# Kernel optimization log

Hardware: AMD Instinct MI355X
Metric: run time of the kernel (lower is better)

Reference implementation:

```python
import jax, jax.numpy as jnp
import numpy as np

N_HEAD = 16


def setup_inputs() -> dict:
    key = jax.random.key(0)
    ks = jax.random.split(key, 5)
    B, S, D = 4, 2048, 1024
    scale = 1.0 / np.sqrt(D)
    return {
        "x": jax.random.normal(ks[0], (B, S, D), dtype=jnp.float32),
        "Wq": jax.random.normal(ks[1], (D, D), dtype=jnp.float32) * scale,
        "bq": jnp.zeros((D,), dtype=jnp.float32),
        "Wk": jax.random.normal(ks[2], (D, D), dtype=jnp.float32) * scale,
        "bk": jnp.zeros((D,), dtype=jnp.float32),
        "Wv": jax.random.normal(ks[3], (D, D), dtype=jnp.float32) * scale,
        "bv": jnp.zeros((D,), dtype=jnp.float32),
        "Wo": jax.random.normal(ks[4], (D, D), dtype=jnp.float32) * scale,
        "bo": jnp.zeros((D,), dtype=jnp.float32),
    }


def reference(x, Wq, bq, Wk, bk, Wv, bv, Wo, bo):
    B, S, D = x.shape
    H = N_HEAD
    Dh = D // H
    # projections (torch Linear == x @ W^T + b; here W stored as (in, out))
    q = (x @ Wq + bq).reshape(B, S, H, Dh).transpose(0, 2, 1, 3)  # (B,H,S,Dh)
    k = (x @ Wk + bk).reshape(B, S, H, Dh).transpose(0, 2, 1, 3)
    v = (x @ Wv + bv).reshape(B, S, H, Dh).transpose(0, 2, 1, 3)
    scores = jnp.einsum("bhsd,bhtd->bhst", q, k) / jnp.sqrt(jnp.float32(Dh))
    causal = jnp.tril(jnp.ones((S, S), dtype=bool))  # (S,S)
    scores = jnp.where(causal[None, None], scores, -jnp.inf)
    weights = jax.nn.softmax(scores, axis=-1)  # (B,H,S,S)
    attn = jnp.einsum("bhst,bhtd->bhsd", weights, v)
    attn = attn.transpose(0, 2, 1, 3).reshape(B, S, D)
    out = attn @ Wo + bo
    return out
```

## Files before the change

### kernel.cpp

```cpp
#include <hip/hip_runtime.h>
#include <hip/hip_bf16.h>


typedef __bf16 bf16x8 __attribute__((ext_vector_type(8)));
typedef float f32x4 __attribute__((ext_vector_type(4)));
typedef unsigned short u16;

__device__ __forceinline__ u16 f2b(float f) {
    __hip_bfloat16 h = __float2bfloat16(f);
    return __builtin_bit_cast(unsigned short, h);
}

__device__ __forceinline__ f32x4 mfma16(bf16x8 a, bf16x8 b, f32x4 c) {
    return __builtin_amdgcn_mfma_f32_16x16x32_bf16(a, b, c, 0, 0, 0);
}

typedef const __attribute__((address_space(1))) unsigned int* gas1_t;
typedef __attribute__((address_space(3))) unsigned int* las3_t;
__device__ __forceinline__ void gld16(const void* g, void* l) {
    __builtin_amdgcn_global_load_lds((gas1_t)g, (las3_t)l, 16, 0, 0);
}

__global__ __launch_bounds__(256) void convert_x(const float* __restrict__ x,
                                                 u16* __restrict__ xb, int n4) {
    int i = blockIdx.x * 256 + threadIdx.x;
    if (i < n4) {
        float4 v = ((const float4*)x)[i];
        ushort4 u;
        u.x = f2b(v.x); u.y = f2b(v.y); u.z = f2b(v.z); u.w = f2b(v.w);
        ((ushort4*)xb)[i] = u;
    }
}

__global__ __launch_bounds__(256) void transpose_w(const float* __restrict__ Wq,
                                                   const float* __restrict__ Wk,
                                                   const float* __restrict__ Wv,
                                                   const float* __restrict__ Wo,
                                                   u16* __restrict__ wqkvt,
                                                   u16* __restrict__ wot) {
    const int z = blockIdx.z;
    const float* src = (z == 0) ? Wq : (z == 1) ? Wk : (z == 2) ? Wv : Wo;
    u16* dst = (z == 3) ? wot : (wqkvt + (size_t)z * 1024 * 1024);
    __shared__ float tile[32][33];
    const int tx = threadIdx.x, ty = threadIdx.y;
    const int nbase = blockIdx.x * 32, kbase = blockIdx.y * 32;
    for (int j = 0; j < 4; ++j)
        tile[ty + j * 8][tx] = src[(size_t)(kbase + ty + j * 8) * 1024 + nbase + tx];
    __syncthreads();
    for (int j = 0; j < 4; ++j)
        dst[(size_t)(nbase + ty + j * 8) * 1024 + kbase + tx] = f2b(tile[tx][ty + j * 8]);
}

__global__ __launch_bounds__(256) void pack_bqkv(const float* __restrict__ bq,
                                                 const float* __restrict__ bk,
                                                 const float* __restrict__ bv,
                                                 float* __restrict__ bqkv) {
    int i = blockIdx.x * 256 + threadIdx.x;
    bqkv[i] = (i < 1024) ? bq[i] : (i < 2048) ? bk[i - 1024] : bv[i - 2048];
}

__global__ __launch_bounds__(512, 2) void gemm256(const u16* __restrict__ A,
                                                  const u16* __restrict__ Bt,
                                                  const float* __restrict__ bias,
                                                  u16* __restrict__ qkout,
                                                  u16* __restrict__ vtout,
                                                  int K) {
    const int tid = threadIdx.x;
    const int l = tid & 63;
    const int w = tid >> 6;
    const int mw = w >> 1;
    const int nw = w & 1;
    const int mrow = l & 15;
    const int tileM = blockIdx.x * 256;
    const int tileN = blockIdx.y * 256;

    __shared__ u16 As[2][2][256 * 32];
    __shared__ u16 Bs[2][2][256 * 32];

    const int rco = ((l >> 4) ^ ((l >> 1) & 3)) * 8;

    const int srow = l >> 2;
    const int scg = (l & 3) ^ ((l >> 3) & 3);
    const u16* aSt = A + (size_t)(tileM + w * 16 + srow) * K + scg * 8;
    const u16* bSt = Bt + (size_t)(tileN + w * 16 + srow) * K + scg * 8;

    f32x4 acc[4][8] = {};

    auto stageAB = [&](int ks, int tt, int nb) {
        const size_t ko = (size_t)(ks * 32 + tt * 64);
        gld16(aSt + ko, &As[nb][ks][(w * 16) * 32]);
        gld16(aSt + (size_t)128 * K + ko, &As[nb][ks][(128 + w * 16) * 32]);
        gld16(bSt + ko, &Bs[nb][ks][(w * 16) * 32]);
        gld16(bSt + (size_t)128 * K + ko, &Bs[nb][ks][(128 + w * 16) * 32]);
    };

    auto phase = [&](int ks, int buf, int tp) {
        asm volatile("s_waitcnt vmcnt(4)" ::: "memory");
        __builtin_amdgcn_s_barrier();
        asm volatile("" ::: "memory");
        bf16x8 aR[4], bR[8];
#pragma unroll
        for (int i = 0; i < 4; ++i) {
            const int r = mw * 64 + i * 16 + mrow;
            aR[i] = *(const bf16x8*)&As[buf][ks][r * 32 + rco];
        }
#pragma unroll
        for (int j = 0; j < 8; ++j) {
            const int r = nw * 128 + j * 16 + mrow;
            bR[j] = *(const bf16x8*)&Bs[buf][ks][r * 32 + rco];
        }
        stageAB(ks, tp, buf ^ 1);
        __builtin_amdgcn_s_setprio(1);
#pragma unroll
        for (int i = 0; i < 4; ++i)
#pragma unroll
            for (int j = 0; j < 8; ++j)
                acc[i][j] = mfma16(aR[i], bR[j], acc[i][j]);
        __builtin_amdgcn_s_setprio(0);
    };

    stageAB(0, 0, 0);
    asm volatile("" ::: "memory");
    stageAB(1, 0, 0);

    const int NT = K >> 6;
    for (int t = 0; t < NT; ++t) {
        const int buf = t & 1;
        const int tp = (t + 1 < NT) ? t + 1 : t;
        phase(0, buf, tp);
        phase(1, buf, tp);
    }
    asm volatile("s_waitcnt vmcnt(0)" ::: "memory");

    const int rbase = (l >> 4) * 4;
#pragma unroll
    for (int i = 0; i < 4; ++i) {
#pragma unroll
        for (int j = 0; j < 8; ++j) {
            const int gm0 = tileM + mw * 64 + i * 16 + rbase;
            const int gn = tileN + nw * 128 + j * 16 + (l & 15);
            const float bv_ = bias[gn];
            const f32x4 a = acc[i][j];
            if (tileN < 2048) {
                const float qs = (tileN < 1024) ? 0.125f * 1.4426950408889634f : 1.0f;
#pragma unroll
                for (int r = 0; r < 4; ++r)
                    qkout[(size_t)(gm0 + r) * 2048 + gn] = f2b((a[r] + bv_) * qs);
            } else {
                const int b = gm0 >> 11, s0 = gm0 & 2047;
                const int gn2 = gn - 2048;
                const int h = gn2 >> 6, dh = gn2 & 63;
                ushort4 u;
                u.x = f2b(a[0] + bv_); u.y = f2b(a[1] + bv_);
                u.z = f2b(a[2] + bv_); u.w = f2b(a[3] + bv_);
                *(ushort4*)&vtout[((size_t)((b * 16 + h) * 64 + dh)) * 2048 + s0] = u;
            }
        }
    }
}

template <int MODE>
__global__ __launch_bounds__(256, 2) void gemm_bt(const u16* __restrict__ A,
                                                  const u16* __restrict__ Bt,
                                                  const float* __restrict__ bias,
                                                  void* __restrict__ Cout,
                                                  void* __restrict__ Cout2,
                                                  int M, int N, int K, int ldc) {
    const int tid = threadIdx.x;
    const int l = tid & 63;
    const int w = tid >> 6;
    const int tileM = blockIdx.x * 128;
    const int tileN = blockIdx.y * 128;

    __shared__ u16 As[2][128 * 32];
    __shared__ u16 Bs[2][128 * 32];

    const int srow = l >> 2;
    const int schunk = l & 3;
    const int mrow = l & 15;
    const int g8 = (l >> 4) * 8;
    const int waveM = (w & 1) * 64;
    const int waveN = (w >> 1) * 64;

    const u16* a0 = A + (size_t)(tileM + w * 32 + srow) * K + schunk * 8;
    const u16* a1 = A + (size_t)(tileM + w * 32 + 16 + srow) * K + schunk * 8;
    const u16* b0 = Bt + (size_t)(tileN + w * 32 + srow) * K + schunk * 8;
    const u16* b1 = Bt + (size_t)(tileN + w * 32 + 16 + srow) * K + schunk * 8;

    f32x4 acc[4][4] = {};

    gld16(a0, &As[0][(w * 2) * 512]);
    gld16(a1, &As[0][(w * 2 + 1) * 512]);
    gld16(b0, &Bs[0][(w * 2) * 512]);
    gld16(b1, &Bs[0][(w * 2 + 1) * 512]);
    __syncthreads();

    for (int k0 = 0; k0 < K; k0 += 32) {
        const int cur = (k0 >> 5) & 1;
        if (k0 + 32 < K) {
            const int nb = cur ^ 1;
            gld16(a0 + k0 + 32, &As[nb][(w * 2) * 512]);
            gld16(a1 + k0 + 32, &As[nb][(w * 2 + 1) * 512]);
            gld16(b0 + k0 + 32, &Bs[nb][(w * 2) * 512]);
            gld16(b1 + k0 + 32, &Bs[nb][(w * 2 + 1) * 512]);
        }

        bf16x8 af[4], bf[4];
        for (int im = 0; im < 4; ++im)
            af[im] = *(const bf16x8*)&As[cur][(waveM + im * 16 + mrow) * 32 + g8];
        for (int in = 0; in < 4; ++in)
            bf[in] = *(const bf16x8*)&Bs[cur][(waveN + in * 16 + mrow) * 32 + g8];
        for (int im = 0; im < 4; ++im)
            for (int in = 0; in < 4; ++in)
                acc[im][in] = mfma16(af[im], bf[in], acc[im][in]);
        __syncthreads();
    }

    const int rbase = (l >> 4) * 4;
    for (int im = 0; im < 4; ++im) {
        for (int in = 0; in < 4; ++in) {
            const int gm0 = tileM + waveM + im * 16 + rbase;
            const int gn = tileN + waveN + in * 16 + (l & 15);
            const float bv_ = bias[gn];
            if (MODE == 1) {
                float* out = (float*)Cout;
                for (int r = 0; r < 4; ++r)
                    out[(size_t)(gm0 + r) * ldc + gn] = acc[im][in][r] + bv_;
            } else if (tileN < 2048) {
                const float qs = (tileN < 1024) ? 0.125f * 1.4426950408889634f : 1.0f;
                u16* out = (u16*)Cout;
                for (int r = 0; r < 4; ++r)
                    out[(size_t)(gm0 + r) * 2048 + gn] = f2b((acc[im][in][r] + bv_) * qs);
            } else {
                u16* out = (u16*)Cout2;
                const int b = gm0 >> 11, s0 = gm0 & 2047;
                const int gn2 = gn - 2048;
                const int h = gn2 >> 6, dh = gn2 & 63;
                ushort4 u;
                u.x = f2b(acc[im][in][0] + bv_);
                u.y = f2b(acc[im][in][1] + bv_);
                u.z = f2b(acc[im][in][2] + bv_);
                u.w = f2b(acc[im][in][3] + bv_);
                *(ushort4*)&out[((size_t)((b * 16 + h) * 64 + dh)) * 2048 + s0] = u;
            }
        }
    }
}

__global__ __launch_bounds__(256, 2) void attn_kernel(const u16* __restrict__ qk,
                                                      const u16* __restrict__ vt,
                                                      u16* __restrict__ attn) {
    const int bh = blockIdx.x;
    const int qt = 15 - (int)blockIdx.y;
    const int b = bh >> 4, h = bh & 15;
    const int q0 = qt * 128;
    const int tid = threadIdx.x, l = tid & 63, w = tid >> 6;
    const int q = l & 15;
    const int g = l >> 4;
    const int g8 = g * 8;

    __shared__ u16 Ks[2][64 * 64];
    __shared__ u16 Vs[2][64 * 64];
    __shared__ u16 Ps[128 * 72];

    const int sr8 = l >> 3;
    const int gc = (l & 7) ^ sr8;
    const u16* kgl = qk + (size_t)(b * 2048 + w * 16 + sr8) * 2048 + 1024 + h * 64 + gc * 8;
    const u16* vgl = vt + (size_t)(bh * 64 + w * 16 + sr8) * 2048 + gc * 8;

    for (int i = 0; i < 4; ++i) {
        const int idx = i * 256 + tid;
        const int row = idx >> 3, ch = idx & 7;
        *(uint4*)&Ps[row * 72 + ch * 8] =
            *(const uint4*)&qk[(size_t)(b * 2048 + q0 + row) * 2048 + h * 64 + ch * 8];
    }
    for (int j = 0; j < 2; ++j) {
        gld16(kgl + (size_t)(j * 8) * 2048, &Ks[0][(w * 16 + j * 8) * 64]);
        gld16(vgl + (size_t)(j * 8) * 2048, &Vs[0][(w * 16 + j * 8) * 64]);
    }
    __syncthreads();

    bf16x8 qb[2][2];
    for (int c = 0; c < 2; ++c) {
        qb[c][0] = *(const bf16x8*)&Ps[(w * 32 + c * 16 + q) * 72 + g8];
        qb[c][1] = *(const bf16x8*)&Ps[(w * 32 + c * 16 + q) * 72 + 32 + g8];
    }

    const int cl0 = ((g) ^ (q & 7)) * 8;
    const int cl1 = ((4 + g) ^ (q & 7)) * 8;

    float li[2] = {0.f, 0.f};
    f32x4 o[2][4] = {};
    const int tmax = 2 * qt + 1;
    const int tdiag = (q0 + w * 32 + 31) >> 6;

    for (int t = 0; t <= tmax; ++t) {
        const int tp = (t < tmax) ? t + 1 : tmax;
        const int nb = (t + 1) & 1;
        for (int j = 0; j < 2; ++j) {
            gld16(kgl + (size_t)(tp * 64 + j * 8) * 2048, &Ks[nb][(w * 16 + j * 8) * 64]);
            gld16(vgl + (size_t)(j * 8) * 2048 + tp * 64, &Vs[nb][(w * 16 + j * 8) * 64]);
        }

        if (t <= tdiag) {
            const int cb0 = t & 1;
            const int kv0 = t * 64;
            const u16* ks = &Ks[cb0][0];
            const u16* vs = &Vs[cb0][0];

            f32x4 st[2][4] = {};
            for (int cb = 0; cb < 4; ++cb) {
                bf16x8 ka0 = *(const bf16x8*)&ks[(cb * 16 + q) * 64 + cl0];
                bf16x8 ka1 = *(const bf16x8*)&ks[(cb * 16 + q) * 64 + cl1];
                st[0][cb] = mfma16(ka0, qb[0][0], st[0][cb]);
                st[1][cb] = mfma16(ka0, qb[1][0], st[1][cb]);
                st[0][cb] = mfma16(ka1, qb[0][1], st[0][cb]);
                st[1][cb] = mfma16(ka1, qb[1][1], st[1][cb]);
            }
            for (int c = 0; c < 2; ++c) {
                if (t == tdiag) {
                    const int qg = q0 + w * 32 + c * 16 + q;
                    for (int cb = 0; cb < 4; ++cb)
                        for (int r = 0; r < 4; ++r) {
                            const int key = kv0 + cb * 16 + g * 4 + r;
                            if (key > qg) st[c][cb][r] = -1e30f;
                        }
                }
                float ps = 0.f;
                for (int cb = 0; cb < 4; ++cb)
                    for (int r = 0; r < 4; ++r) {
                        const float p = __builtin_amdgcn_exp2f(st[c][cb][r]);
                        st[c][cb][r] = p;
                        ps += p;
                    }
                li[c] += ps;
                for (int cb = 0; cb < 4; ++cb) {
                    ushort4 u;
                    u.x = f2b(st[c][cb][0]); u.y = f2b(st[c][cb][1]);
                    u.z = f2b(st[c][cb][2]); u.w = f2b(st[c][cb][3]);
                    *(ushort4*)&Ps[(w * 32 + c * 16 + q) * 72 + cb * 16 + g * 4] = u;
                }
            }
            __builtin_amdgcn_s_waitcnt(0xC07F);
            for (int cb = 0; cb < 4; ++cb) {
                bf16x8 va0 = *(const bf16x8*)&vs[(cb * 16 + q) * 64 + cl0];
                bf16x8 va1 = *(const bf16x8*)&vs[(cb * 16 + q) * 64 + cl1];
                bf16x8 pb00 = *(const bf16x8*)&Ps[(w * 32 + q) * 72 + g8];
                bf16x8 pb01 = *(const bf16x8*)&Ps[(w * 32 + q) * 72 + 32 + g8];
                bf16x8 pb10 = *(const bf16x8*)&Ps[(w * 32 + 16 + q) * 72 + g8];
                bf16x8 pb11 = *(const bf16x8*)&Ps[(w * 32 + 16 + q) * 72 + 32 + g8];
                o[0][cb] = mfma16(va0, pb00, o[0][cb]);
                o[1][cb] = mfma16(va0, pb10, o[1][cb]);
                o[0][cb] = mfma16(va1, pb01, o[0][cb]);
                o[1][cb] = mfma16(va1, pb11, o[1][cb]);
            }
        }
        __syncthreads();
    }

    for (int c = 0; c < 2; ++c) {
        float ps = li[c];
        ps += __shfl_xor(ps, 16);
        ps += __shfl_xor(ps, 32);
        const float inv = 1.0f / ps;
        const size_t tok = (size_t)(b * 2048 + q0 + w * 32 + c * 16 + q);
        for (int cb = 0; cb < 4; ++cb) {
            ushort4 u;
            u.x = f2b(o[c][cb][0] * inv); u.y = f2b(o[c][cb][1] * inv);
            u.z = f2b(o[c][cb][2] * inv); u.w = f2b(o[c][cb][3] * inv);
            *(ushort4*)&attn[tok * 1024 + h * 64 + cb * 16 + g * 4] = u;
        }
    }
}

extern "C" void kernel_launch(void* const* d_in, const int* in_sizes, int n_in,
                              void* d_out, int out_size, void* d_ws, size_t ws_size,
                              hipStream_t stream) {
    const float* x  = (const float*)d_in[0];
    const float* Wq = (const float*)d_in[1];
    const float* bq = (const float*)d_in[2];
    const float* Wk = (const float*)d_in[3];
    const float* bk = (const float*)d_in[4];
    const float* Wv = (const float*)d_in[5];
    const float* bv = (const float*)d_in[6];
    const float* Wo = (const float*)d_in[7];
    const float* bo = (const float*)d_in[8];
    float* out = (float*)d_out;

    char* ws = (char*)d_ws;
    size_t off = 0;
    auto alloc = [&](size_t bytes) -> void* {
        void* p = ws + off;
        off += (bytes + 255) & ~(size_t)255;
        return p;
    };
    u16*   xb    = (u16*)alloc(8192ull * 1024 * 2);
    u16*   wqkvt = (u16*)alloc(3072ull * 1024 * 2);
    u16*   wot   = (u16*)alloc(1024ull * 1024 * 2);
    float* bqkv  = (float*)alloc(3072ull * 4);
    u16*   qk    = (u16*)alloc(8192ull * 2048 * 2);
    u16*   vt    = (u16*)alloc(8192ull * 1024 * 2);
    u16*   attn  = (u16*)alloc(8192ull * 1024 * 2);

    convert_x<<<8192, 256, 0, stream>>>(x, xb, 8192 * 1024 / 4);
    transpose_w<<<dim3(32, 32, 4), dim3(32, 8), 0, stream>>>(Wq, Wk, Wv, Wo, wqkvt, wot);
    pack_bqkv<<<12, 256, 0, stream>>>(bq, bk, bv, bqkv);
    gemm256<<<dim3(32, 12), 512, 0, stream>>>(xb, wqkvt, bqkv, qk, vt, 1024);
    attn_kernel<<<dim3(64, 16), 256, 0, stream>>>(qk, vt, attn);
    gemm_bt<1><<<dim3(64, 8), 256, 0, stream>>>(attn, wot, bo, out, nullptr, 8192, 1024, 1024, 1024);
}
```

Before: 254.2 us.

## Retile QKV GEMM waves to 2x4 and interleave LDS reads with MFMAs

Reorganizes the QKV projection GEMM so each wave computes a 128x64 subtile from a 2x4 wave grid. Each K step now uses a single 64-wide stage with a new XOR swizzle. Fragment loads and the next-tile prefetch are split into chunks interleaved with MFMA groups, with one barrier per 64-k step. The aim is to cut barrier count and hide LDS and global latency behind matrix math. The cost is higher register pressure from the held fragments and reliance on __syncthreads to drain the async loads.

```diff
diff --git a/kernel.cpp b/kernel.cpp
--- a/kernel.cpp
+++ b/kernel.cpp
@@ -68,77 +68,92 @@
     const int tid = threadIdx.x;
     const int l = tid & 63;
     const int w = tid >> 6;
-    const int mw = w >> 1;
-    const int nw = w & 1;
-    const int mrow = l & 15;
+    const int mw2 = w >> 2;
+    const int nw4 = w & 3;
     const int tileM = blockIdx.x * 256;
     const int tileN = blockIdx.y * 256;
 
-    __shared__ u16 As[2][2][256 * 32];
-    __shared__ u16 Bs[2][2][256 * 32];
-
-    const int rco = ((l >> 4) ^ ((l >> 1) & 3)) * 8;
-
-    const int srow = l >> 2;
-    const int scg = (l & 3) ^ ((l >> 3) & 3);
-    const u16* aSt = A + (size_t)(tileM + w * 16 + srow) * K + scg * 8;
-    const u16* bSt = Bt + (size_t)(tileN + w * 16 + srow) * K + scg * 8;
-
-    f32x4 acc[4][8] = {};
-
-    auto stageAB = [&](int ks, int tt, int nb) {
-        const size_t ko = (size_t)(ks * 32 + tt * 64);
-        gld16(aSt + ko, &As[nb][ks][(w * 16) * 32]);
-        gld16(aSt + (size_t)128 * K + ko, &As[nb][ks][(128 + w * 16) * 32]);
-        gld16(bSt + ko, &Bs[nb][ks][(w * 16) * 32]);
-        gld16(bSt + (size_t)128 * K + ko, &Bs[nb][ks][(128 + w * 16) * 32]);
+    __shared__ u16 As[2][256 * 64];
+    __shared__ u16 Bs[2][256 * 64];
+
+    const int co0 = (((l >> 4)) ^ (l & 7)) * 8;
+    const int co1 = ((4 + (l >> 4)) ^ (l & 7)) * 8;
+    const int mrow = l & 15;
+
+    const int sro = l >> 3;
+    const int scg = (l & 7) ^ sro;
+    const u16* aSt = A + (size_t)(tileM + w * 16 + sro) * K + scg * 8;
+    const u16* bSt = Bt + (size_t)(tileN + w * 16 + sro) * K + scg * 8;
+
+    f32x4 acc[8][4] = {};
+    bf16x8 aR[4][2];
+    bf16x8 bR[4][2];
+
+    auto stage = [&](int mat, int h, int tt, int nb) {
+        const size_t go = (size_t)h * 128 * K + (size_t)tt * 64;
+        u16* lb = (mat ? &Bs[nb][0] : &As[nb][0]) + (h * 128 + w * 16) * 64;
+        const u16* gp = (mat ? bSt : aSt) + go;
+        gld16(gp, lb);
+        gld16(gp + (size_t)8 * K, lb + 8 * 64);
     };
-
-    auto phase = [&](int ks, int buf, int tp) {
-        asm volatile("s_waitcnt vmcnt(4)" ::: "memory");
-        __builtin_amdgcn_s_barrier();
-        asm volatile("" ::: "memory");
-        bf16x8 aR[4], bR[8];
+    auto loadA = [&](int mh, int buf) {
 #pragma unroll
         for (int i = 0; i < 4; ++i) {
-            const int r = mw * 64 + i * 16 + mrow;
-            aR[i] = *(const bf16x8*)&As[buf][ks][r * 32 + rco];
-        }
-#pragma unroll
-        for (int j = 0; j < 8; ++j) {
-            const int r = nw * 128 + j * 16 + mrow;
-            bR[j] = *(const bf16x8*)&Bs[buf][ks][r * 32 + rco];
-        }
-        stageAB(ks, tp, buf ^ 1);
+            const int r = mw2 * 128 + mh * 64 + i * 16 + mrow;
+            aR[i][0] = *(const bf16x8*)&As[buf][r * 64 + co0];
+            aR[i][1] = *(const bf16x8*)&As[buf][r * 64 + co1];
+        }
+    };
+    auto loadB = [&](int nh, int buf) {
+#pragma unroll
+        for (int j = 0; j < 2; ++j) {
+            const int r = nw4 * 64 + nh * 32 + j * 16 + mrow;
+            bR[nh * 2 + j][0] = *(const bf16x8*)&Bs[buf][r * 64 + co0];
+            bR[nh * 2 + j][1] = *(const bf16x8*)&Bs[buf][r * 64 + co1];
+        }
+    };
+    auto mm = [&](int mi0, int nj0) {
         __builtin_amdgcn_s_setprio(1);
 #pragma unroll
-        for (int i = 0; i < 4; ++i)
-#pragma unroll
-            for (int j = 0; j < 8; ++j)
-                acc[i][j] = mfma16(aR[i], bR[j], acc[i][j]);
+        for (int ks = 0; ks < 2; ++ks)
+#pragma unroll
+            for (int i = 0; i < 4; ++i)
+#pragma unroll
+                for (int j = 0; j < 2; ++j)
+                    acc[mi0 + i][nj0 + j] =
+                        mfma16(aR[i][ks], bR[nj0 + j][ks], acc[mi0 + i][nj0 + j]);
         __builtin_amdgcn_s_setprio(0);
     };
 
-    stageAB(0, 0, 0);
-    asm volatile("" ::: "memory");
-    stageAB(1, 0, 0);
+    stage(0, 0, 0, 0); stage(0, 1, 0, 0); stage(1, 0, 0, 0); stage(1, 1, 0, 0);
 
     const int NT = K >> 6;
     for (int t = 0; t < NT; ++t) {
-        const int buf = t & 1;
-        const int tp = (t + 1 < NT) ? t + 1 : t;
-        phase(0, buf, tp);
-        phase(1, buf, tp);
-    }
-    asm volatile("s_waitcnt vmcnt(0)" ::: "memory");
+        const int buf = t & 1, nb = buf ^ 1;
+        const bool pf = (t + 1 < NT);
+        __syncthreads();
+
+        loadA(0, buf);
+        loadB(0, buf);
+        if (pf) stage(0, 0, t + 1, nb);
+        mm(0, 0);
+        loadB(1, buf);
+        if (pf) stage(0, 1, t + 1, nb);
+        mm(0, 2);
+        loadA(1, buf);
+        if (pf) stage(1, 0, t + 1, nb);
+        mm(4, 2);
+        if (pf) stage(1, 1, t + 1, nb);
+        mm(4, 0);
+    }
 
     const int rbase = (l >> 4) * 4;
 #pragma unroll
-    for (int i = 0; i < 4; ++i) {
-#pragma unroll
-        for (int j = 0; j < 8; ++j) {
-            const int gm0 = tileM + mw * 64 + i * 16 + rbase;
-            const int gn = tileN + nw * 128 + j * 16 + (l & 15);
+    for (int i = 0; i < 8; ++i) {
+#pragma unroll
+        for (int j = 0; j < 4; ++j) {
+            const int gm0 = tileM + mw2 * 128 + i * 16 + rbase;
+            const int gn = tileN + nw4 * 64 + j * 16 + (l & 15);
             const float bv_ = bias[gn];
             const f32x4 a = acc[i][j];
             if (tileN < 2048) {
```

Result: faster. 244.7 us (-3.8%).
